# Kernel tuning notes

Hardware: AMD Instinct MI355X
Metric: run time of the kernel (lower is better)

Reference implementation:

```python
import jax, jax.numpy as jnp
import numpy as np

RESO = 32          # grid_resolution
HID = 32           # hidden_dim
CDIM = 32          # c_dim
NBLK = 5           # n_blocks
PAD = 0.1          # padding
L = 10             # positional encoding frequencies -> dim 60


def setup_inputs() -> dict:
    key = jax.random.key(0)
    ks = jax.random.split(key, 12)
    B, T = 2, 200000
    p = jax.random.uniform(ks[0], (B, T, 3), jnp.float32, -0.5, 0.5)
    s = 0.05
    return {
        "p": p,
        "fc_pos_w": jax.random.normal(ks[1], (60, 2 * HID), jnp.float32) * s,
        "fc_pos_b": jax.random.normal(ks[2], (2 * HID,), jnp.float32) * s,
        "blk_fc0_w": jax.random.normal(ks[3], (NBLK, 2 * HID, HID), jnp.float32) * s,
        "blk_fc0_b": jax.random.normal(ks[4], (NBLK, HID), jnp.float32) * s,
        "blk_fc1_w": jax.random.normal(ks[5], (NBLK, HID, HID), jnp.float32) * s,
        "blk_fc1_b": jax.random.normal(ks[6], (NBLK, HID), jnp.float32) * s,
        "blk_sc_w": jax.random.normal(ks[7], (NBLK, 2 * HID, HID), jnp.float32) * s,  # shortcut, no bias
        "fc_c_w": jax.random.normal(ks[8], (HID, CDIM), jnp.float32) * s,
        "fc_c_b": jax.random.normal(ks[9], (CDIM,), jnp.float32) * s,
    }


def _pos_encode(p):
    # p in [-0.5,0.5] -> [-2,0] after 2p-1 (matches torch impl: p = 2*p - 1)
    q = 2.0 * p - 1.0
    freqs = (jnp.pi * (2.0 ** jnp.arange(L, dtype=jnp.float32)))  # [L]
    a = q[..., None, :] * freqs[:, None]                          # [B,T,L,3]
    pe = jnp.stack([jnp.sin(a), jnp.cos(a)], axis=-2)             # [B,T,L,2,3]
    return pe.reshape(*p.shape[:-1], 2 * L * 3)                   # [B,T,60]


def _normalize_3d(p):
    p_nor = p / (1.0 + PAD + 1e-3) + 0.5
    return jnp.clip(p_nor, 0.0, 1.0 - 1e-3)


def _coord2index(p_nor):
    x = jnp.floor(p_nor * RESO).astype(jnp.int32)                  # [B,T,3]
    return x[..., 0] + RESO * (x[..., 1] + RESO * x[..., 2])       # [B,T]


def _resblock(x, w0, b0, w1, b1, ws):
    h = jax.nn.relu(jax.nn.relu(x) @ w0 + b0)
    return x @ ws + (jax.nn.relu(h) @ w1 + b1)


def reference(p, fc_pos_w, fc_pos_b, blk_fc0_w, blk_fc0_b, blk_fc1_w, blk_fc1_b,
              blk_sc_w, fc_c_w, fc_c_b):
    B, T, _ = p.shape
    G = RESO ** 3
    p_nor = _normalize_3d(p)
    idx = _coord2index(p_nor)                                      # [B,T]
    gidx = (idx + jnp.arange(B, dtype=jnp.int32)[:, None] * G).reshape(-1)  # [B*T]

    net = _pos_encode(p) @ fc_pos_w + fc_pos_b                     # [B,T,64]
    net = _resblock(net, blk_fc0_w[0], blk_fc0_b[0], blk_fc1_w[0], blk_fc1_b[0], blk_sc_w[0])
    for i in range(1, NBLK):
        # pool_local: scatter_max per grid cell, gather back to points
        flat = net.reshape(B * T, HID)
        cell = jax.ops.segment_max(flat, gidx, num_segments=B * G)  # [B*G,HID]
        pooled = cell[gidx].reshape(B, T, HID)
        net = jnp.concatenate([net, pooled], axis=-1)               # [B,T,64]
        net = _resblock(net, blk_fc0_w[i], blk_fc0_b[i], blk_fc1_w[i], blk_fc1_b[i], blk_sc_w[i])

    c = net @ fc_c_w + fc_c_b                                       # [B,T,CDIM]

    # generate_grid_features: scatter_mean into grid (empty cells = 0)
    cf = c.reshape(B * T, CDIM)
    sums = jax.ops.segment_sum(cf, gidx, num_segments=B * G)        # [B*G,CDIM]
    cnt = jax.ops.segment_sum(jnp.ones((B * T, 1), c.dtype), gidx, num_segments=B * G)
    mean = sums / jnp.maximum(cnt, 1.0)
    fea_grid = mean.reshape(B, G, CDIM).transpose(0, 2, 1).reshape(B, CDIM, RESO, RESO, RESO)
    return fea_grid
```

## Files before the change

kernel.cpp:

```cpp
#include <hip/hip_runtime.h>
#include <math.h>

#define TPTS 200000
#define BB 2
#define NPTS (BB*TPTS)
#define GRID3 32768
#define BG 65536
#define SROWS 176

typedef __attribute__((ext_vector_type(8))) __bf16 bf16x8;
typedef __attribute__((ext_vector_type(4))) float f32x4;
typedef unsigned short ushort_t;

#define MFMA16(a,b,c) __builtin_amdgcn_mfma_f32_16x16x32_bf16(a,b,c,0,0,0)

__device__ __forceinline__ void split8(const float* v, bf16x8& hi, bf16x8& lo)
{
#pragma unroll
  for (int j = 0; j < 8; j++) {
    float f = v[j];
    __bf16 h = (__bf16)f;
    hi[j] = h;
    lo[j] = (__bf16)(f - (float)h);
  }
}

__device__ __forceinline__ int cellof(float p0, float p1, float p2, int t)
{
  const float DEN = (float)(1.0 + 0.1 + 1e-3);
  const float HI  = (float)(1.0 - 1e-3);
  float n0 = fminf(fmaxf(p0/DEN + 0.5f, 0.f), HI);
  float n1 = fminf(fmaxf(p1/DEN + 0.5f, 0.f), HI);
  float n2 = fminf(fmaxf(p2/DEN + 0.5f, 0.f), HI);
  int c0 = (int)floorf(n0*32.f), c1 = (int)floorf(n1*32.f), c2 = (int)floorf(n2*32.f);
  return c0 + 32*(c1 + 32*c2) + (t >= TPTS ? GRID3 : 0);
}

__global__ __launch_bounds__(256) void k_hist(
    const float* __restrict__ p, int* __restrict__ gbuf, int* __restrict__ hist)
{
  int t = blockIdx.x*256 + threadIdx.x;
  if (t >= NPTS) return;
  int g = cellof(p[3*t], p[3*t+1], p[3*t+2], t);
  gbuf[t] = g;
  atomicAdd(hist + g, 1);
}

__global__ __launch_bounds__(256) void k_scanA(
    const int* __restrict__ hist, int* __restrict__ texcl, int* __restrict__ bsum)
{
  __shared__ int sm[256];
  int tid = threadIdx.x;
  int t = blockIdx.x*256 + tid;
  int v = hist[t];
  sm[tid] = v; __syncthreads();
  for (int off = 1; off < 256; off <<= 1) {
    int x = sm[tid];
    int u = (tid >= off) ? sm[tid-off] : 0;
    __syncthreads();
    sm[tid] = x + u;
    __syncthreads();
  }
  texcl[t] = sm[tid] - v;
  if (tid == 255) bsum[blockIdx.x] = sm[255];
}

__global__ __launch_bounds__(256) void k_scanB(
    const int* __restrict__ bsum, int* __restrict__ boff)
{
  __shared__ int sm[256];
  int tid = threadIdx.x;
  int v = bsum[tid];
  sm[tid] = v; __syncthreads();
  for (int off = 1; off < 256; off <<= 1) {
    int x = sm[tid];
    int u = (tid >= off) ? sm[tid-off] : 0;
    __syncthreads();
    sm[tid] = x + u;
    __syncthreads();
  }
  boff[tid] = sm[tid] - v;
}

__global__ __launch_bounds__(256) void k_scanC(
    const int* __restrict__ texcl, const int* __restrict__ boff,
    int* __restrict__ start, int* __restrict__ cursor)
{
  int t = blockIdx.x*256 + threadIdx.x;
  int v = boff[blockIdx.x] + texcl[t];
  start[t] = v; cursor[t] = v;
  if (t == 0) start[BG] = NPTS;
}

__global__ __launch_bounds__(256) void k_scatter(
    const float* __restrict__ p, const int* __restrict__ gbuf,
    int* __restrict__ cursor, float* __restrict__ p_sorted, int* __restrict__ gsort)
{
  int t = blockIdx.x*256 + threadIdx.x;
  if (t >= NPTS) return;
  int g = gbuf[t];
  int slot = atomicAdd(cursor + g, 1);
  gsort[slot] = g;
  p_sorted[3*slot]   = p[3*t];
  p_sorted[3*slot+1] = p[3*t+1];
  p_sorted[3*slot+2] = p[3*t+2];
}

__global__ void k_pack(
    const float* __restrict__ f0w, const float* __restrict__ scw,
    const float* __restrict__ f1w, const float* __restrict__ wc,
    const float* __restrict__ Wp,
    ushort_t* __restrict__ wpack)
{
  int f = blockIdx.x, l = threadIdx.x;
  if (f >= 104) {
    int idx = f - 104;
    int c = idx >> 3, t = (idx >> 1) & 3, e = idx & 1;
#pragma unroll
    for (int j = 0; j < 8; j++) {
      int k = c*32 + (l>>4)*8 + j, n = t*16 + (l&15);
      float v = (k < 60) ? Wp[k*64 + n] : 0.f;
      __bf16 h = (__bf16)v;
      __bf16 out = (e == 0) ? h : (__bf16)(v - (float)h);
      union { __bf16 b; ushort_t u; } cv; cv.b = out;
      wpack[((size_t)f*64 + l)*8 + j] = cv.u;
    }
    return;
  }
  const float* W; int c, t, e;
  if (f < 100) {
    int s = f / 20, r = f % 20;
    if (r < 8)       { W = f0w + s*2048; c = r>>2;        t = (r>>1)&1; e = r&1; }
    else if (r < 16) { int q = r-8;  W = scw + s*2048; c = q>>2; t = (q>>1)&1; e = q&1; }
    else             { int q = r-16; W = f1w + s*1024; c = 0;    t = q>>1;     e = q&1; }
  } else { int q = f-100; W = wc; c = 0; t = q>>1; e = q&1; }
#pragma unroll
  for (int j = 0; j < 8; j++) {
    int k = c*32 + (l>>4)*8 + j, n = t*16 + (l&15);
    float v = W[k*32 + n];
    __bf16 h = (__bf16)v;
    __bf16 out = (e == 0) ? h : (__bf16)(v - (float)h);
    union { __bf16 b; ushort_t u; } cv; cv.b = out;
    wpack[((size_t)f*64 + l)*8 + j] = cv.u;
  }
}

__global__ __launch_bounds__(256) void k_fused0(
    const float* __restrict__ ps,
    const ushort_t* __restrict__ wpPE, const float* __restrict__ bp,
    const ushort_t* __restrict__ wp,
    const float* __restrict__ b0, const float* __restrict__ b1,
    float* __restrict__ net)
{
  __shared__ float xlds[4][16*68];
  __shared__ float hbuf[4][16*36];
  int wave = threadIdx.x >> 6, lane = threadIdx.x & 63;
  int m = lane & 15, q = lane >> 4;
  int pbase = (blockIdx.x*4 + wave)*16;
  int pt = pbase + m;

  float p0 = ps[3*pt], p1 = ps[3*pt+1], p2 = ps[3*pt+2];
  float u0 = 2.f*p0 - 1.f, u1 = 2.f*p1 - 1.f, u2 = 2.f*p2 - 1.f;
  const float PIF = 3.14159265358979323846f;

  float pe[2][8];
#pragma unroll
  for (int c2 = 0; c2 < 2; c2++) {
#pragma unroll
    for (int jj = 0; jj < 8; jj++) {
      int e = c2*32 + q*8 + jj;
      int l = (e * 43691) >> 18;
      int r = e - l*6;
      bool issin = (r < 3);
      int d = issin ? r : (r - 3);
      float ud = (d == 0) ? u0 : ((d == 1) ? u1 : u2);
      float xval = ldexpf(ud, l);
      float red = xval - 2.f*rintf(0.5f*xval);
      float ang = PIF*red + (issin ? 0.f : 1.5707963267948966f);
      float v = __sinf(ang);
      pe[c2][jj] = (e < 60) ? v : 0.f;
    }
  }
  bf16x8 peh[2], pel[2];
  split8(pe[0], peh[0], pel[0]);
  split8(pe[1], peh[1], pel[1]);

  f32x4 xacc[4];
#pragma unroll
  for (int t = 0; t < 4; t++) {
    float bb = bp[t*16 + m];
    xacc[t] = (f32x4){bb,bb,bb,bb};
  }
#pragma unroll
  for (int c2 = 0; c2 < 2; c2++)
#pragma unroll
    for (int t = 0; t < 4; t++) {
      bf16x8 bh = *(const bf16x8*)(wpPE + ((size_t)((c2*4+t)*2    )*64 + lane)*8);
      bf16x8 bl = *(const bf16x8*)(wpPE + ((size_t)((c2*4+t)*2 + 1)*64 + lane)*8);
      xacc[t] = MFMA16(peh[c2], bh, xacc[t]);
      xacc[t] = MFMA16(pel[c2], bh, xacc[t]);
      xacc[t] = MFMA16(peh[c2], bl, xacc[t]);
    }

  float* xl = xlds[wave];
#pragma unroll
  for (int t = 0; t < 4; t++)
#pragma unroll
    for (int r = 0; r < 4; r++)
      xl[(q*4+r)*68 + t*16 + m] = xacc[t][r];
  __syncthreads();

  float xv[2][8];
#pragma unroll
  for (int c2 = 0; c2 < 2; c2++)
#pragma unroll
    for (int jj = 0; jj < 8; jj++)
      xv[c2][jj] = xl[m*68 + c2*32 + q*8 + jj];

  bf16x8 w0f[2][2][2], wsf[2][2][2], w1f[2][2];
#pragma unroll
  for (int c = 0; c < 2; c++)
#pragma unroll
    for (int t = 0; t < 2; t++)
#pragma unroll
      for (int e = 0; e < 2; e++) {
        w0f[c][t][e] = *(const bf16x8*)(wp + ((size_t)(((c*2+t)*2+e)    )*64 + lane)*8);
        wsf[c][t][e] = *(const bf16x8*)(wp + ((size_t)(((c*2+t)*2+e) + 8)*64 + lane)*8);
      }
#pragma unroll
  for (int t = 0; t < 2; t++)
#pragma unroll
    for (int e = 0; e < 2; e++)
      w1f[t][e] = *(const bf16x8*)(wp + ((size_t)(16 + t*2 + e)*64 + lane)*8);

  bf16x8 axh[2], axl[2], arh[2], arl[2];
#pragma unroll
  for (int c = 0; c < 2; c++) {
    float r[8];
#pragma unroll
    for (int j = 0; j < 8; j++) r[j] = fmaxf(xv[c][j], 0.f);
    split8(xv[c], axh[c], axl[c]);
    split8(r,     arh[c], arl[c]);
  }

  f32x4 hacc[2], yacc[2];
#pragma unroll
  for (int t = 0; t < 2; t++) {
    float bb0 = b0[m + 16*t], bb1 = b1[m + 16*t];
    hacc[t] = (f32x4){bb0,bb0,bb0,bb0};
    yacc[t] = (f32x4){bb1,bb1,bb1,bb1};
  }

#pragma unroll
  for (int c = 0; c < 2; c++)
#pragma unroll
    for (int t = 0; t < 2; t++) {
      hacc[t] = MFMA16(arh[c], w0f[c][t][0], hacc[t]);
      hacc[t] = MFMA16(arl[c], w0f[c][t][0], hacc[t]);
      hacc[t] = MFMA16(arh[c], w0f[c][t][1], hacc[t]);
      yacc[t] = MFMA16(axh[c], wsf[c][t][0], yacc[t]);
      yacc[t] = MFMA16(axl[c], wsf[c][t][0], yacc[t]);
      yacc[t] = MFMA16(axh[c], wsf[c][t][1], yacc[t]);
    }

  float* hb = hbuf[wave];
#pragma unroll
  for (int t = 0; t < 2; t++)
#pragma unroll
    for (int r = 0; r < 4; r++)
      hb[(q*4+r)*36 + m + 16*t] = fmaxf(hacc[t][r], 0.f);
  __syncthreads();
  float hv[8];
#pragma unroll
  for (int j = 0; j < 8; j++) hv[j] = hb[m*36 + q*8 + j];
  bf16x8 hh, hl; split8(hv, hh, hl);
#pragma unroll
  for (int t = 0; t < 2; t++) {
    yacc[t] = MFMA16(hh, w1f[t][0], yacc[t]);
    yacc[t] = MFMA16(hl, w1f[t][0], yacc[t]);
    yacc[t] = MFMA16(hh, w1f[t][1], yacc[t]);
  }

#pragma unroll
  for (int t = 0; t < 2; t++)
#pragma unroll
    for (int r = 0; r < 4; r++)
      net[(size_t)(pbase + q*4 + r)*32 + m + 16*t] = yacc[t][r];
}

__global__ __launch_bounds__(256) void k_stage_f(
    const float* __restrict__ netin, float* __restrict__ netout,
    const int* __restrict__ gsort, const int* __restrict__ start,
    const ushort_t* __restrict__ wp,
    const float* __restrict__ b0, const float* __restrict__ b1)
{
  __shared__ float sbuf[SROWS*36];
  int tid = threadIdx.x;
  int P0 = blockIdx.x*64;
  int s = start[gsort[P0]];
  int e = start[gsort[P0+63] + 1];
  int n = e - s; if (n > SROWS) n = SROWS;

  for (int idx = tid; idx < n*8; idx += 256) {
    int r = idx >> 3, c = idx & 7;
    *(f32x4*)(sbuf + r*36 + c*4) =
      *(const f32x4*)(netin + ((size_t)(s + r))*32 + c*4);
  }
  __syncthreads();

  int wave = tid >> 6, lane = tid & 63;
  int m = lane & 15, q = lane >> 4;
  int pbase = P0 + wave*16;
  int pt = pbase + m;
  int g = gsort[pt];
  int cs = start[g] - s, ce = start[g+1] - s;

  float xv[2][8];
  {
    const float* xr = sbuf + (pt - s)*36 + q*8;
    *(f32x4*)&xv[0][0] = *(const f32x4*)xr;
    *(f32x4*)&xv[0][4] = *(const f32x4*)(xr + 4);
  }
  {
    f32x4 ma = (f32x4){-INFINITY,-INFINITY,-INFINITY,-INFINITY};
    f32x4 mb = ma;
    for (int k = cs; k < ce; k++) {
      const float* rr = sbuf + k*36 + q*8;
      f32x4 va = *(const f32x4*)rr;
      f32x4 vb = *(const f32x4*)(rr + 4);
      ma.x = fmaxf(ma.x, va.x); ma.y = fmaxf(ma.y, va.y);
      ma.z = fmaxf(ma.z, va.z); ma.w = fmaxf(ma.w, va.w);
      mb.x = fmaxf(mb.x, vb.x); mb.y = fmaxf(mb.y, vb.y);
      mb.z = fmaxf(mb.z, vb.z); mb.w = fmaxf(mb.w, vb.w);
    }
    *(f32x4*)&xv[1][0] = ma;
    *(f32x4*)&xv[1][4] = mb;
  }

  bf16x8 w0f[2][2][2], wsf[2][2][2], w1f[2][2];
#pragma unroll
  for (int c = 0; c < 2; c++)
#pragma unroll
    for (int t = 0; t < 2; t++)
#pragma unroll
      for (int e2 = 0; e2 < 2; e2++) {
        w0f[c][t][e2] = *(const bf16x8*)(wp + ((size_t)(((c*2+t)*2+e2)    )*64 + lane)*8);
        wsf[c][t][e2] = *(const bf16x8*)(wp + ((size_t)(((c*2+t)*2+e2) + 8)*64 + lane)*8);
      }
#pragma unroll
  for (int t = 0; t < 2; t++)
#pragma unroll
    for (int e2 = 0; e2 < 2; e2++)
      w1f[t][e2] = *(const bf16x8*)(wp + ((size_t)(16 + t*2 + e2)*64 + lane)*8);

  bf16x8 axh[2], axl[2], arh[2], arl[2];
#pragma unroll
  for (int c = 0; c < 2; c++) {
    float r[8];
#pragma unroll
    for (int j = 0; j < 8; j++) r[j] = fmaxf(xv[c][j], 0.f);
    split8(xv[c], axh[c], axl[c]);
    split8(r,     arh[c], arl[c]);
  }

  f32x4 hacc[2], yacc[2];
#pragma unroll
  for (int t = 0; t < 2; t++) {
    float bb0 = b0[m + 16*t], bb1 = b1[m + 16*t];
    hacc[t] = (f32x4){bb0,bb0,bb0,bb0};
    yacc[t] = (f32x4){bb1,bb1,bb1,bb1};
  }

#pragma unroll
  for (int c = 0; c < 2; c++)
#pragma unroll
    for (int t = 0; t < 2; t++) {
      hacc[t] = MFMA16(arh[c], w0f[c][t][0], hacc[t]);
      hacc[t] = MFMA16(arl[c], w0f[c][t][0], hacc[t]);
      hacc[t] = MFMA16(arh[c], w0f[c][t][1], hacc[t]);
      yacc[t] = MFMA16(axh[c], wsf[c][t][0], yacc[t]);
      yacc[t] = MFMA16(axl[c], wsf[c][t][0], yacc[t]);
      yacc[t] = MFMA16(axh[c], wsf[c][t][1], yacc[t]);
    }

  __syncthreads();
  float* hb = sbuf + wave*576;
#pragma unroll
  for (int t = 0; t < 2; t++)
#pragma unroll
    for (int r = 0; r < 4; r++)
      hb[(q*4+r)*36 + m + 16*t] = fmaxf(hacc[t][r], 0.f);
  __syncthreads();
  float hv[8];
#pragma unroll
  for (int j = 0; j < 8; j++) hv[j] = hb[m*36 + q*8 + j];
  bf16x8 hh, hl; split8(hv, hh, hl);
#pragma unroll
  for (int t = 0; t < 2; t++) {
    yacc[t] = MFMA16(hh, w1f[t][0], yacc[t]);
    yacc[t] = MFMA16(hl, w1f[t][0], yacc[t]);
    yacc[t] = MFMA16(hh, w1f[t][1], yacc[t]);
  }

#pragma unroll
  for (int t = 0; t < 2; t++)
#pragma unroll
    for (int r = 0; r < 4; r++)
      netout[(size_t)(pbase + q*4 + r)*32 + m + 16*t] = yacc[t][r];
}

__global__ __launch_bounds__(256) void k_final_f(
    const float* __restrict__ netin, float* __restrict__ netout,
    const int* __restrict__ gsort, const int* __restrict__ start,
    const ushort_t* __restrict__ wp, const ushort_t* __restrict__ wpc,
    const float* __restrict__ b0, const float* __restrict__ b1,
    const float* __restrict__ bc)
{
  __shared__ float sbuf[SROWS*36];
  int tid = threadIdx.x;
  int P0 = blockIdx.x*64;
  int s = start[gsort[P0]];
  int e = start[gsort[P0+63] + 1];
  int n = e - s; if (n > SROWS) n = SROWS;

  for (int idx = tid; idx < n*8; idx += 256) {
    int r = idx >> 3, c = idx & 7;
    *(f32x4*)(sbuf + r*36 + c*4) =
      *(const f32x4*)(netin + ((size_t)(s + r))*32 + c*4);
  }
  __syncthreads();

  int wave = tid >> 6, lane = tid & 63;
  int m = lane & 15, q = lane >> 4;
  int pbase = P0 + wave*16;
  int pt = pbase + m;
  int g = gsort[pt];
  int cs = start[g] - s, ce = start[g+1] - s;

  float xv[2][8];
  {
    const float* xr = sbuf + (pt - s)*36 + q*8;
    *(f32x4*)&xv[0][0] = *(const f32x4*)xr;
    *(f32x4*)&xv[0][4] = *(const f32x4*)(xr + 4);
  }
  {
    f32x4 ma = (f32x4){-INFINITY,-INFINITY,-INFINITY,-INFINITY};
    f32x4 mb = ma;
    for (int k = cs; k < ce; k++) {
      const float* rr = sbuf + k*36 + q*8;
      f32x4 va = *(const f32x4*)rr;
      f32x4 vb = *(const f32x4*)(rr + 4);
      ma.x = fmaxf(ma.x, va.x); ma.y = fmaxf(ma.y, va.y);
      ma.z = fmaxf(ma.z, va.z); ma.w = fmaxf(ma.w, va.w);
      mb.x = fmaxf(mb.x, vb.x); mb.y = fmaxf(mb.y, vb.y);
      mb.z = fmaxf(mb.z, vb.z); mb.w = fmaxf(mb.w, vb.w);
    }
    *(f32x4*)&xv[1][0] = ma;
    *(f32x4*)&xv[1][4] = mb;
  }

  bf16x8 w0f[2][2][2], wsf[2][2][2], w1f[2][2], wcf[2][2];
#pragma unroll
  for (int c = 0; c < 2; c++)
#pragma unroll
    for (int t = 0; t < 2; t++)
#pragma unroll
      for (int e2 = 0; e2 < 2; e2++) {
        w0f[c][t][e2] = *(const bf16x8*)(wp + ((size_t)(((c*2+t)*2+e2)    )*64 + lane)*8);
        wsf[c][t][e2] = *(const bf16x8*)(wp + ((size_t)(((c*2+t)*2+e2) + 8)*64 + lane)*8);
      }
#pragma unroll
  for (int t = 0; t < 2; t++)
#pragma unroll
    for (int e2 = 0; e2 < 2; e2++) {
      w1f[t][e2] = *(const bf16x8*)(wp  + ((size_t)(16 + t*2 + e2)*64 + lane)*8);
      wcf[t][e2] = *(const bf16x8*)(wpc + ((size_t)(     t*2 + e2)*64 + lane)*8);
    }

  bf16x8 axh[2], axl[2], arh[2], arl[2];
#pragma unroll
  for (int c = 0; c < 2; c++) {
    float r[8];
#pragma unroll
    for (int j = 0; j < 8; j++) r[j] = fmaxf(xv[c][j], 0.f);
    split8(xv[c], axh[c], axl[c]);
    split8(r,     arh[c], arl[c]);
  }

  f32x4 hacc[2], yacc[2];
#pragma unroll
  for (int t = 0; t < 2; t++) {
    float bb0 = b0[m + 16*t], bb1 = b1[m + 16*t];
    hacc[t] = (f32x4){bb0,bb0,bb0,bb0};
    yacc[t] = (f32x4){bb1,bb1,bb1,bb1};
  }

#pragma unroll
  for (int c = 0; c < 2; c++)
#pragma unroll
    for (int t = 0; t < 2; t++) {
      hacc[t] = MFMA16(arh[c], w0f[c][t][0], hacc[t]);
      hacc[t] = MFMA16(arl[c], w0f[c][t][0], hacc[t]);
      hacc[t] = MFMA16(arh[c], w0f[c][t][1], hacc[t]);
      yacc[t] = MFMA16(axh[c], wsf[c][t][0], yacc[t]);
      yacc[t] = MFMA16(axl[c], wsf[c][t][0], yacc[t]);
      yacc[t] = MFMA16(axh[c], wsf[c][t][1], yacc[t]);
    }

  __syncthreads();
  float* hb = sbuf + wave*576;
  float* yb = sbuf + 4*576 + wave*576;
#pragma unroll
  for (int t = 0; t < 2; t++)
#pragma unroll
    for (int r = 0; r < 4; r++)
      hb[(q*4+r)*36 + m + 16*t] = fmaxf(hacc[t][r], 0.f);
  __syncthreads();
  float hv[8];
#pragma unroll
  for (int j = 0; j < 8; j++) hv[j] = hb[m*36 + q*8 + j];
  bf16x8 hh, hl; split8(hv, hh, hl);
#pragma unroll
  for (int t = 0; t < 2; t++) {
    yacc[t] = MFMA16(hh, w1f[t][0], yacc[t]);
    yacc[t] = MFMA16(hl, w1f[t][0], yacc[t]);
    yacc[t] = MFMA16(hh, w1f[t][1], yacc[t]);
  }

#pragma unroll
  for (int t = 0; t < 2; t++)
#pragma unroll
    for (int r = 0; r < 4; r++)
      yb[(q*4+r)*36 + m + 16*t] = yacc[t][r];
  __syncthreads();
  float yv[8];
#pragma unroll
  for (int j = 0; j < 8; j++) yv[j] = yb[m*36 + q*8 + j];
  bf16x8 yh, yl; split8(yv, yh, yl);

  f32x4 cacc[2];
#pragma unroll
  for (int t = 0; t < 2; t++) {
    float bb = bc[m + 16*t];
    cacc[t] = (f32x4){bb,bb,bb,bb};
    cacc[t] = MFMA16(yh, wcf[t][0], cacc[t]);
    cacc[t] = MFMA16(yl, wcf[t][0], cacc[t]);
    cacc[t] = MFMA16(yh, wcf[t][1], cacc[t]);
  }

#pragma unroll
  for (int t = 0; t < 2; t++)
#pragma unroll
    for (int r = 0; r < 4; r++)
      netout[(size_t)(pbase + q*4 + r)*32 + m + 16*t] = cacc[t][r];
}

__global__ __launch_bounds__(256) void k_mean(
    const float* __restrict__ net, const int* __restrict__ start,
    float* __restrict__ outp)
{
  int tid = blockIdx.x*256 + threadIdx.x;
  int c = tid >> 3, sub = tid & 7;
  int s = start[c], e = start[c+1];
  f32x4 sum = (f32x4){0.f,0.f,0.f,0.f};
  for (int k = s; k < e; k++) {
    f32x4 v = *(const f32x4*)(net + (size_t)k*32 + sub*4);
    sum.x += v.x; sum.y += v.y; sum.z += v.z; sum.w += v.w;
  }
  float inv = (e > s) ? 1.f/(float)(e - s) : 0.f;
  int b = c >> 15, cell = c & 32767;
  size_t ob = ((size_t)b << 20) + cell;
#pragma unroll
  for (int jj = 0; jj < 4; jj++) {
    int ch = sub*4 + jj;
    float v = ((const float*)&sum)[jj] * inv;
    outp[ob + ((size_t)ch << 15)] = v;
  }
}

extern "C" void kernel_launch(void* const* d_in, const int* in_sizes, int n_in,
                              void* d_out, int out_size, void* d_ws, size_t ws_size,
                              hipStream_t stream)
{
  const float* p   = (const float*)d_in[0];
  const float* Wp  = (const float*)d_in[1];
  const float* bp  = (const float*)d_in[2];
  const float* f0w = (const float*)d_in[3];
  const float* f0b = (const float*)d_in[4];
  const float* f1w = (const float*)d_in[5];
  const float* f1b = (const float*)d_in[6];
  const float* scw = (const float*)d_in[7];
  const float* wc  = (const float*)d_in[8];
  const float* bc  = (const float*)d_in[9];
  float* outp = (float*)d_out;

  char* wsb = (char*)d_ws;
  float*    netA     = (float*)wsb;
  float*    netB     = netA + (size_t)NPTS*32;
  int*      gbuf     = (int*)(netB + (size_t)NPTS*32);
  int*      gsort    = gbuf + NPTS;
  int*      hist     = gsort + NPTS;
  int*      start    = hist + BG;
  int*      cursor   = start + BG + 1;
  int*      texcl    = cursor + BG;
  int*      bsum     = texcl + BG;
  int*      boff     = bsum + 256;
  ushort_t* wpack    = (ushort_t*)(boff + 256);
  float*    p_sorted = (float*)(wpack + (size_t)120*512);

  dim3 blk(256);
  dim3 gpts((NPTS + 255)/256);
  dim3 gmfma(NPTS/64);
  dim3 gcell((BG*8)/256);
  dim3 gscan(BG/256);

  hipMemsetAsync(hist, 0, (size_t)BG*4, stream);
  hipLaunchKernelGGL(k_hist, gpts, blk, 0, stream, p, gbuf, hist);
  hipLaunchKernelGGL(k_scanA, gscan, blk, 0, stream, hist, texcl, bsum);
  hipLaunchKernelGGL(k_scanB, dim3(1), blk, 0, stream, bsum, boff);
  hipLaunchKernelGGL(k_scanC, gscan, blk, 0, stream, texcl, boff, start, cursor);
  hipLaunchKernelGGL(k_scatter, gpts, blk, 0, stream, p, gbuf, cursor, p_sorted, gsort);
  hipLaunchKernelGGL(k_pack, dim3(120), dim3(64), 0, stream, f0w, scw, f1w, wc, Wp, wpack);
  hipLaunchKernelGGL(k_fused0, gmfma, blk, 0, stream,
                     p_sorted, wpack + (size_t)104*512, bp,
                     wpack + (size_t)0*20*512, f0b + 0*32, f1b + 0*32, netA);
  hipLaunchKernelGGL(k_stage_f, gmfma, blk, 0, stream, netA, netB, gsort, start,
                     wpack + (size_t)1*20*512, f0b + 1*32, f1b + 1*32);
  hipLaunchKernelGGL(k_stage_f, gmfma, blk, 0, stream, netB, netA, gsort, start,
                     wpack + (size_t)2*20*512, f0b + 2*32, f1b + 2*32);
  hipLaunchKernelGGL(k_stage_f, gmfma, blk, 0, stream, netA, netB, gsort, start,
                     wpack + (size_t)3*20*512, f0b + 3*32, f1b + 3*32);
  hipLaunchKernelGGL(k_final_f, gmfma, blk, 0, stream, netB, netA, gsort, start,
                     wpack + (size_t)4*20*512, wpack + (size_t)100*512,
                     f0b + 4*32, f1b + 4*32, bc);
  hipLaunchKernelGGL(k_mean, gcell, blk, 0, stream, netA, start, outp);
}
```

Before: 331.4 us.

## Replace per-point cell max loop with LDS atomic max and fuse scatter-mean into final stage

The pool stages now reduce each cell once, using order-preserving integer atomicMax into LDS slots, instead of having every point loop over its whole cell. The point's own features are read from global memory rather than staged in LDS. The final stage accumulates per-cell sums in LDS and atomically adds them into the zeroed output grid. A small scale kernel then divides by the count, which removes the separate mean pass and the write-back of the per-point features. This adds LDS and global atomics and an output memset, and relies on rowslot mapping each row to its cell's first row.

```diff
diff --git a/kernel.cpp b/kernel.cpp
--- a/kernel.cpp
+++ b/kernel.cpp
@@ -7,6 +7,7 @@
 #define GRID3 32768
 #define BG 65536
 #define SROWS 176
+#define SLOTSTR 40
 
 typedef __attribute__((ext_vector_type(8))) __bf16 bf16x8;
 typedef __attribute__((ext_vector_type(4))) float f32x4;
@@ -23,6 +24,17 @@
     hi[j] = h;
     lo[j] = (__bf16)(f - (float)h);
   }
+}
+
+__device__ __forceinline__ int ordenc(float f)
+{
+  int b = __float_as_int(f);
+  return b ^ ((b >> 31) & 0x7fffffff);
+}
+__device__ __forceinline__ float orddec(int k)
+{
+  int b = k ^ ((k >> 31) & 0x7fffffff);
+  return __int_as_float(b);
 }
 
 __device__ __forceinline__ int cellof(float p0, float p1, float p2, int t)
@@ -294,17 +306,28 @@
     const ushort_t* __restrict__ wp,
     const float* __restrict__ b0, const float* __restrict__ b1)
 {
-  __shared__ float sbuf[SROWS*36];
+  __shared__ int slots[SROWS*SLOTSTR];
+  __shared__ int rowslot[SROWS];
   int tid = threadIdx.x;
   int P0 = blockIdx.x*64;
   int s = start[gsort[P0]];
   int e = start[gsort[P0+63] + 1];
   int n = e - s; if (n > SROWS) n = SROWS;
 
+  for (int r = tid; r < n; r += 256)
+    rowslot[r] = start[gsort[s + r]] - s;
+  for (int i = tid; i < n*32; i += 256)
+    slots[(i>>5)*SLOTSTR + (i&31)] = (int)0x80000000;
+  __syncthreads();
+
   for (int idx = tid; idx < n*8; idx += 256) {
-    int r = idx >> 3, c = idx & 7;
-    *(f32x4*)(sbuf + r*36 + c*4) =
-      *(const f32x4*)(netin + ((size_t)(s + r))*32 + c*4);
+    int r = idx >> 3, c4 = idx & 7;
+    f32x4 v = *(const f32x4*)(netin + (size_t)(s + r)*32 + c4*4);
+    int base = rowslot[r]*SLOTSTR + c4*4;
+    atomicMax(&slots[base+0], ordenc(v.x));
+    atomicMax(&slots[base+1], ordenc(v.y));
+    atomicMax(&slots[base+2], ordenc(v.z));
+    atomicMax(&slots[base+3], ordenc(v.w));
   }
   __syncthreads();
 
@@ -312,29 +335,18 @@
   int m = lane & 15, q = lane >> 4;
   int pbase = P0 + wave*16;
   int pt = pbase + m;
-  int g = gsort[pt];
-  int cs = start[g] - s, ce = start[g+1] - s;
 
   float xv[2][8];
   {
-    const float* xr = sbuf + (pt - s)*36 + q*8;
+    const float* xr = netin + (size_t)pt*32 + q*8;
     *(f32x4*)&xv[0][0] = *(const f32x4*)xr;
     *(f32x4*)&xv[0][4] = *(const f32x4*)(xr + 4);
   }
   {
-    f32x4 ma = (f32x4){-INFINITY,-INFINITY,-INFINITY,-INFINITY};
-    f32x4 mb = ma;
-    for (int k = cs; k < ce; k++) {
-      const float* rr = sbuf + k*36 + q*8;
-      f32x4 va = *(const f32x4*)rr;
-      f32x4 vb = *(const f32x4*)(rr + 4);
-      ma.x = fmaxf(ma.x, va.x); ma.y = fmaxf(ma.y, va.y);
-      ma.z = fmaxf(ma.z, va.z); ma.w = fmaxf(ma.w, va.w);
-      mb.x = fmaxf(mb.x, vb.x); mb.y = fmaxf(mb.y, vb.y);
-      mb.z = fmaxf(mb.z, vb.z); mb.w = fmaxf(mb.w, vb.w);
-    }
-    *(f32x4*)&xv[1][0] = ma;
-    *(f32x4*)&xv[1][4] = mb;
+    int srow = rowslot[pt - s];
+    const int* sp = slots + srow*SLOTSTR + q*8;
+#pragma unroll
+    for (int j = 0; j < 8; j++) xv[1][j] = orddec(sp[j]);
   }
 
   bf16x8 w0f[2][2][2], wsf[2][2][2], w1f[2][2];
@@ -384,7 +396,8 @@
     }
 
   __syncthreads();
-  float* hb = sbuf + wave*576;
+  float* fs = (float*)slots;
+  float* hb = fs + wave*576;
 #pragma unroll
   for (int t = 0; t < 2; t++)
 #pragma unroll
@@ -410,23 +423,35 @@
 }
 
 __global__ __launch_bounds__(256) void k_final_f(
-    const float* __restrict__ netin, float* __restrict__ netout,
+    const float* __restrict__ netin,
     const int* __restrict__ gsort, const int* __restrict__ start,
     const ushort_t* __restrict__ wp, const ushort_t* __restrict__ wpc,
     const float* __restrict__ b0, const float* __restrict__ b1,
-    const float* __restrict__ bc)
-{
-  __shared__ float sbuf[SROWS*36];
+    const float* __restrict__ bc,
+    float* __restrict__ outp)
+{
+  __shared__ int slots[SROWS*SLOTSTR];
+  __shared__ int rowslot[SROWS];
   int tid = threadIdx.x;
   int P0 = blockIdx.x*64;
   int s = start[gsort[P0]];
   int e = start[gsort[P0+63] + 1];
   int n = e - s; if (n > SROWS) n = SROWS;
 
+  for (int r = tid; r < n; r += 256)
+    rowslot[r] = start[gsort[s + r]] - s;
+  for (int i = tid; i < n*32; i += 256)
+    slots[(i>>5)*SLOTSTR + (i&31)] = (int)0x80000000;
+  __syncthreads();
+
   for (int idx = tid; idx < n*8; idx += 256) {
-    int r = idx >> 3, c = idx & 7;
-    *(f32x4*)(sbuf + r*36 + c*4) =
-      *(const f32x4*)(netin + ((size_t)(s + r))*32 + c*4);
+    int r = idx >> 3, c4 = idx & 7;
+    f32x4 v = *(const f32x4*)(netin + (size_t)(s + r)*32 + c4*4);
+    int base = rowslot[r]*SLOTSTR + c4*4;
+    atomicMax(&slots[base+0], ordenc(v.x));
+    atomicMax(&slots[base+1], ordenc(v.y));
+    atomicMax(&slots[base+2], ordenc(v.z));
+    atomicMax(&slots[base+3], ordenc(v.w));
   }
   __syncthreads();
 
@@ -434,29 +459,18 @@
   int m = lane & 15, q = lane >> 4;
   int pbase = P0 + wave*16;
   int pt = pbase + m;
-  int g = gsort[pt];
-  int cs = start[g] - s, ce = start[g+1] - s;
 
   float xv[2][8];
   {
-    const float* xr = sbuf + (pt - s)*36 + q*8;
+    const float* xr = netin + (size_t)pt*32 + q*8;
     *(f32x4*)&xv[0][0] = *(const f32x4*)xr;
     *(f32x4*)&xv[0][4] = *(const f32x4*)(xr + 4);
   }
   {
-    f32x4 ma = (f32x4){-INFINITY,-INFINITY,-INFINITY,-INFINITY};
-    f32x4 mb = ma;
-    for (int k = cs; k < ce; k++) {
-      const float* rr = sbuf + k*36 + q*8;
-      f32x4 va = *(const f32x4*)rr;
-      f32x4 vb = *(const f32x4*)(rr + 4);
-      ma.x = fmaxf(ma.x, va.x); ma.y = fmaxf(ma.y, va.y);
-      ma.z = fmaxf(ma.z, va.z); ma.w = fmaxf(ma.w, va.w);
-      mb.x = fmaxf(mb.x, vb.x); mb.y = fmaxf(mb.y, vb.y);
-      mb.z = fmaxf(mb.z, vb.z); mb.w = fmaxf(mb.w, vb.w);
-    }
-    *(f32x4*)&xv[1][0] = ma;
-    *(f32x4*)&xv[1][4] = mb;
+    int srow = rowslot[pt - s];
+    const int* sp = slots + srow*SLOTSTR + q*8;
+#pragma unroll
+    for (int j = 0; j < 8; j++) xv[1][j] = orddec(sp[j]);
   }
 
   bf16x8 w0f[2][2][2], wsf[2][2][2], w1f[2][2], wcf[2][2];
@@ -508,8 +522,9 @@
     }
 
   __syncthreads();
-  float* hb = sbuf + wave*576;
-  float* yb = sbuf + 4*576 + wave*576;
+  float* fs = (float*)slots;
+  float* hb = fs + wave*576;
+  float* yb = fs + 4*576 + wave*576;
 #pragma unroll
   for (int t = 0; t < 2; t++)
 #pragma unroll
@@ -548,34 +563,46 @@
     cacc[t] = MFMA16(yh, wcf[t][1], cacc[t]);
   }
 
-#pragma unroll
-  for (int t = 0; t < 2; t++)
-#pragma unroll
-    for (int r = 0; r < 4; r++)
-      netout[(size_t)(pbase + q*4 + r)*32 + m + 16*t] = cacc[t][r];
-}
-
-__global__ __launch_bounds__(256) void k_mean(
-    const float* __restrict__ net, const int* __restrict__ start,
-    float* __restrict__ outp)
-{
-  int tid = blockIdx.x*256 + threadIdx.x;
-  int c = tid >> 3, sub = tid & 7;
-  int s = start[c], e = start[c+1];
-  f32x4 sum = (f32x4){0.f,0.f,0.f,0.f};
-  for (int k = s; k < e; k++) {
-    f32x4 v = *(const f32x4*)(net + (size_t)k*32 + sub*4);
-    sum.x += v.x; sum.y += v.y; sum.z += v.z; sum.w += v.w;
-  }
-  float inv = (e > s) ? 1.f/(float)(e - s) : 0.f;
-  int b = c >> 15, cell = c & 32767;
-  size_t ob = ((size_t)b << 20) + cell;
-#pragma unroll
-  for (int jj = 0; jj < 4; jj++) {
-    int ch = sub*4 + jj;
-    float v = ((const float*)&sum)[jj] * inv;
-    outp[ob + ((size_t)ch << 15)] = v;
-  }
+  __syncthreads();
+  for (int i = tid; i < n*32; i += 256)
+    fs[(i>>5)*SLOTSTR + (i&31)] = 0.f;
+  __syncthreads();
+#pragma unroll
+  for (int r = 0; r < 4; r++) {
+    int srow = rowslot[pbase + q*4 + r - s];
+#pragma unroll
+    for (int t = 0; t < 2; t++)
+      atomicAdd(fs + srow*SLOTSTR + m + 16*t, cacc[t][r]);
+  }
+  __syncthreads();
+
+  {
+    int o = tid >> 2, c4 = tid & 3;
+    int r = (P0 - s) + o;
+    int rs = rowslot[r];
+    if (o == 0 || rs == r) {
+      int g = gsort[P0 + o];
+      int b = g >> 15, cell = g & 32767;
+      float* ob = outp + ((size_t)b << 20) + cell;
+      const float* sv = fs + rs*SLOTSTR;
+#pragma unroll
+      for (int j = 0; j < 8; j++) {
+        int ch = c4*8 + j;
+        atomicAdd(ob + ((size_t)ch << 15), sv[ch]);
+      }
+    }
+  }
+}
+
+__global__ __launch_bounds__(256) void k_scale(
+    float* __restrict__ outp, const int* __restrict__ start)
+{
+  int i = blockIdx.x*256 + threadIdx.x;
+  int cell = i & 32767;
+  int b = i >> 20;
+  int g = (b << 15) | cell;
+  int cnt = start[g+1] - start[g];
+  if (cnt > 1) outp[i] = outp[i] / (float)cnt;
 }
 
 extern "C" void kernel_launch(void* const* d_in, const int* in_sizes, int n_in,
@@ -611,10 +638,11 @@
   dim3 blk(256);
   dim3 gpts((NPTS + 255)/256);
   dim3 gmfma(NPTS/64);
-  dim3 gcell((BG*8)/256);
   dim3 gscan(BG/256);
+  dim3 gscale((BG*32)/256);
 
   hipMemsetAsync(hist, 0, (size_t)BG*4, stream);
+  hipMemsetAsync(outp, 0, (size_t)BG*32*4, stream);
   hipLaunchKernelGGL(k_hist, gpts, blk, 0, stream, p, gbuf, hist);
   hipLaunchKernelGGL(k_scanA, gscan, blk, 0, stream, hist, texcl, bsum);
   hipLaunchKernelGGL(k_scanB, dim3(1), blk, 0, stream, bsum, boff);
@@ -630,8 +658,8 @@
                      wpack + (size_t)2*20*512, f0b + 2*32, f1b + 2*32);
   hipLaunchKernelGGL(k_stage_f, gmfma, blk, 0, stream, netA, netB, gsort, start,
                      wpack + (size_t)3*20*512, f0b + 3*32, f1b + 3*32);
-  hipLaunchKernelGGL(k_final_f, gmfma, blk, 0, stream, netB, netA, gsort, start,
+  hipLaunchKernelGGL(k_final_f, gmfma, blk, 0, stream, netB, gsort, start,
                      wpack + (size_t)4*20*512, wpack + (size_t)100*512,
-                     f0b + 4*32, f1b + 4*32, bc);
-  hipLaunchKernelGGL(k_mean, gcell, blk, 0, stream, netA, start, outp);
-}
+                     f0b + 4*32, f1b + 4*32, bc, outp);
+  hipLaunchKernelGGL(k_scale, gscale, blk, 0, stream, outp, start);
+}
```

Result: slower. 399.4 us (+20.5%).
